# Optimization experiments

Measured on AMD Instinct MI355X. Metric: run time of the kernel, lower is better.

## Reference

```python
import jax, jax.numpy as jnp
import numpy as np

B, S, D, E, K = 4, 2048, 1024, 8, 2
LN_EPS = 1e-5


def setup_inputs() -> dict:
    key = jax.random.key(0)
    ks = jax.random.split(key, 8)
    s = 1.0 / np.sqrt(D)
    return {
        "x": jax.random.normal(ks[0], (B, S, D), dtype=jnp.float32),
        "noise": jax.random.normal(ks[1], (B, S, E), dtype=jnp.float32) * (1.0 / E),
        "W_route": jax.random.uniform(ks[2], (D, E), minval=-s, maxval=s, dtype=jnp.float32),
        "b_route": jax.random.uniform(ks[3], (E,), minval=-s, maxval=s, dtype=jnp.float32),
        "ln_gamma": jnp.ones((E,), dtype=jnp.float32),
        "ln_beta": jnp.zeros((E,), dtype=jnp.float32),
        "W_exp": jax.random.uniform(ks[4], (E, D, D), minval=-s, maxval=s, dtype=jnp.float32),
        "b_exp": jax.random.uniform(ks[5], (E, D), minval=-s, maxval=s, dtype=jnp.float32),
    }


def reference(x, noise, W_route, b_route, ln_gamma, ln_beta, W_exp, b_exp):
    # Routing: Linear(dim, E) -> LayerNorm(E) -> softmax, plus noise
    logits = jnp.einsum("bsd,de->bse", x, W_route) + b_route
    mu = logits.mean(axis=-1, keepdims=True)
    var = logits.var(axis=-1, keepdims=True)
    ln = (logits - mu) / jnp.sqrt(var + LN_EPS) * ln_gamma + ln_beta
    routing = jax.nn.softmax(ln, axis=-1) + noise

    topk_w, topk_i = jax.lax.top_k(routing, K)          # [B,S,K]
    topk_w = jax.nn.softmax(topk_w, axis=-1)

    # Dense all-expert compute (faithful to the naive original)
    expert_out = jnp.einsum("bsd,edf->bsef", x, W_exp) + b_exp  # [B,S,E,D]

    # Gather top-k experts per token and combine
    sel = jnp.take_along_axis(expert_out, topk_i[..., None], axis=2)  # [B,S,K,D]
    return (sel * topk_w[..., None]).sum(axis=2)
```

## Files before the change

### kernel.cpp

```cpp
#include <hip/hip_runtime.h>
#include <hip/hip_bf16.h>


typedef unsigned short u16;
typedef __bf16 bf16x8 __attribute__((ext_vector_type(8)));
typedef float floatx4 __attribute__((ext_vector_type(4)));
typedef unsigned short u16x8 __attribute__((ext_vector_type(8)));

#define NTOK 8192
#define DDIM 1024
#define NEXP 8

__device__ __forceinline__ u16 f2bf(float f) {
    union { float f; unsigned int i; } c; c.f = f;
    unsigned int i = c.i;
    return (u16)((i + 0x7fffu + ((i >> 16) & 1u)) >> 16);
}

__device__ __forceinline__ int swz(int row, int chunk) {
    return row * 32 + ((chunk ^ ((row >> 1) & 3)) << 3);
}

__global__ __launch_bounds__(256) void xcast(const float* __restrict__ x,
                                             u16* __restrict__ xb) {
    size_t i = ((size_t)blockIdx.x * 256 + threadIdx.x) * 8;
    float4 a = *(const float4*)(x + i);
    float4 b = *(const float4*)(x + i + 4);
    u16x8 v;
    v[0] = f2bf(a.x); v[1] = f2bf(a.y); v[2] = f2bf(a.z); v[3] = f2bf(a.w);
    v[4] = f2bf(b.x); v[5] = f2bf(b.y); v[6] = f2bf(b.z); v[7] = f2bf(b.w);
    *(u16x8*)(xb + i) = v;
}

__global__ __launch_bounds__(256) void transpose_w(const float* __restrict__ W,
                                                   u16* __restrict__ WT) {
    __shared__ __align__(16) u16 tile[64][72];
    const int e = blockIdx.z, d0 = blockIdx.y * 64, f0 = blockIdx.x * 64;
    const int t = threadIdx.x;
    const float* src = W + (size_t)e * DDIM * DDIM;
    u16* dst = WT + (size_t)e * DDIM * DDIM;
#pragma unroll
    for (int it = 0; it < 2; ++it) {
        int idx = it * 256 + t;
        int r = idx >> 3, c8 = idx & 7;
        const float* sp = src + (size_t)(d0 + r) * DDIM + f0 + c8 * 8;
        float4 va = *(const float4*)sp;
        float4 vb = *(const float4*)(sp + 4);
        u16x8 v;
        v[0] = f2bf(va.x); v[1] = f2bf(va.y); v[2] = f2bf(va.z); v[3] = f2bf(va.w);
        v[4] = f2bf(vb.x); v[5] = f2bf(vb.y); v[6] = f2bf(vb.z); v[7] = f2bf(vb.w);
        *(u16x8*)&tile[r][c8 * 8] = v;
    }
    __syncthreads();
#pragma unroll
    for (int it = 0; it < 2; ++it) {
        int idx = it * 256 + t;
        int fr = idx >> 3, d8 = idx & 7;
        u16x8 o;
#pragma unroll
        for (int j = 0; j < 8; ++j) o[j] = tile[d8 * 8 + j][fr];
        *(u16x8*)(dst + (size_t)(f0 + fr) * DDIM + d0 + d8 * 8) = o;
    }
}

__global__ __launch_bounds__(256) void routing_compute(
    const float* __restrict__ x, const float* __restrict__ noise,
    const float* __restrict__ Wr, const float* __restrict__ br,
    const float* __restrict__ gamma, const float* __restrict__ beta,
    int* __restrict__ e01, float2* __restrict__ w01) {
    __shared__ __align__(16) float wrT[NEXP][DDIM];
    const int t = threadIdx.x;
#pragma unroll
    for (int i = 0; i < 8; ++i) {
        int f4 = i * 256 + t;
        int d = f4 >> 1, half = (f4 & 1) * 4;
        float4 v = *(const float4*)&Wr[d * 8 + half];
        wrT[half + 0][d] = v.x; wrT[half + 1][d] = v.y;
        wrT[half + 2][d] = v.z; wrT[half + 3][d] = v.w;
    }
    __syncthreads();

    const int wave = t >> 6, lane = t & 63;
    const int tok = blockIdx.x * 4 + wave;
    const float4* xrow = (const float4*)(x + (size_t)tok * DDIM);
    float acc[8];
#pragma unroll
    for (int e = 0; e < 8; ++e) acc[e] = 0.f;
#pragma unroll
    for (int i = 0; i < 4; ++i) {
        int d4 = i * 64 + lane;
        float4 xv = xrow[d4];
#pragma unroll
        for (int e = 0; e < 8; ++e) {
            float4 wv = *(const float4*)&wrT[e][d4 * 4];
            acc[e] += xv.x * wv.x + xv.y * wv.y + xv.z * wv.z + xv.w * wv.w;
        }
    }
#pragma unroll
    for (int off = 32; off >= 1; off >>= 1) {
#pragma unroll
        for (int e = 0; e < 8; ++e) acc[e] += __shfl_xor(acc[e], off, 64);
    }
    if (lane == 0) {
        float lg[8], mu = 0.f;
#pragma unroll
        for (int e = 0; e < 8; ++e) { lg[e] = acc[e] + br[e]; mu += lg[e]; }
        mu *= 0.125f;
        float var = 0.f;
#pragma unroll
        for (int e = 0; e < 8; ++e) { float d = lg[e] - mu; var += d * d; }
        var *= 0.125f;
        float rstd = rsqrtf(var + 1e-5f);
        float ln[8], mx = -1e30f;
#pragma unroll
        for (int e = 0; e < 8; ++e) {
            ln[e] = (lg[e] - mu) * rstd * gamma[e] + beta[e];
            mx = fmaxf(mx, ln[e]);
        }
        float s = 0.f, p[8];
#pragma unroll
        for (int e = 0; e < 8; ++e) { p[e] = expf(ln[e] - mx); s += p[e]; }
        float inv = 1.f / s, r[8];
#pragma unroll
        for (int e = 0; e < 8; ++e) r[e] = p[e] * inv + noise[(size_t)tok * 8 + e];
        int i0 = 0; float v0 = r[0];
#pragma unroll
        for (int e = 1; e < 8; ++e) if (r[e] > v0) { v0 = r[e]; i0 = e; }
        int i1 = -1; float v1 = -1e30f;
#pragma unroll
        for (int e = 0; e < 8; ++e) if (e != i0 && r[e] > v1) { v1 = r[e]; i1 = e; }
        float w0 = 1.f / (1.f + expf(v1 - v0));
        e01[tok] = i0 | (i1 << 8);
        w01[tok] = make_float2(w0, 1.f - w0);
    }
}

__global__ __launch_bounds__(256) void build_lists(
    const int* __restrict__ e01, const float2* __restrict__ w01,
    int* __restrict__ counts, int* __restrict__ list_tok, float* __restrict__ list_w) {
    const int g = blockIdx.x;
    const int slot = g >> 3, ex = g & 7;
    const int t = threadIdx.x, wave = t >> 6, lane = t & 63;
    __shared__ int wtot[4];
    int base = 0;
    for (int start = 0; start < NTOK; start += 256) {
        int tok = start + t;
        int packed = e01[tok];
        int e = slot ? ((packed >> 8) & 0xff) : (packed & 0xff);
        bool sel = (e == ex);
        unsigned long long m = __ballot(sel);
        int prefix = __popcll(m & ((1ULL << lane) - 1ULL));
        if (lane == 0) wtot[wave] = __popcll(m);
        __syncthreads();
        int wbase = 0;
#pragma unroll
        for (int wv = 0; wv < 4; ++wv) if (wv < wave) wbase += wtot[wv];
        int total = wtot[0] + wtot[1] + wtot[2] + wtot[3];
        if (sel) {
            float2 w2 = w01[tok];
            int pos = base + wbase + prefix;
            list_tok[g * NTOK + pos] = tok;
            list_w[g * NTOK + pos] = slot ? w2.y : w2.x;
        }
        base += total;
        __syncthreads();
    }
    if (t == 0) counts[g] = base;
}

template <int BF16A>
__global__ __launch_bounds__(256) void moe_gemm(
    const float* __restrict__ xf, const u16* __restrict__ xb,
    const u16* __restrict__ WT, const float* __restrict__ bexp,
    const int* __restrict__ counts, const int* __restrict__ list_tok,
    const float* __restrict__ list_w, float* __restrict__ out,
    int grp_base, int accum) {
    const int e = blockIdx.z;
    const int grp = grp_base + e;
    int cnt = counts[grp];
    cnt = cnt < 0 ? 0 : (cnt > NTOK ? NTOK : cnt);
    const int lin = blockIdx.x;
    const int n = (lin >> 3) & 7;
    const int m = (lin & 7) | ((lin >> 6) << 3);
    const int m0 = m * 128;
    if (m0 >= cnt) return;
    const int n0 = n * 128;

    __shared__ __align__(16) u16 A_s[128 * 32];
    __shared__ __align__(16) u16 B_s[128 * 32];
    __shared__ int tok_s[128];
    __shared__ float w_s[128];
    __shared__ float bias_s[128];

    const int t = threadIdx.x;
    if (t < 128) {
        int r = m0 + t;
        int rr = r < cnt ? r : cnt - 1;
        tok_s[t] = list_tok[grp * NTOK + rr] & (NTOK - 1);
        w_s[t] = (r < cnt) ? list_w[grp * NTOK + rr] : 0.f;
        bias_s[t] = bexp[e * DDIM + n0 + t];
    }
    __syncthreads();

    const int ra = t >> 2;
    const int ch = t & 3;
    const int co = ch * 8;
    const u16* wg0 = WT + ((size_t)e * DDIM + n0 + ra) * DDIM + co;
    const u16* wg1 = WT + ((size_t)e * DDIM + n0 + 64 + ra) * DDIM + co;
    u16* sA0 = A_s + swz(ra, ch);
    u16* sA1 = A_s + swz(64 + ra, ch);
    u16* sB0 = B_s + swz(ra, ch);
    u16* sB1 = B_s + swz(64 + ra, ch);

    const int lane = t & 63, wave = t >> 6;
    const int wm = wave >> 1, wn = wave & 1;
    const int lm = lane & 15;
    const int kc = lane >> 4;

    floatx4 acc[4][4];
#pragma unroll
    for (int mi = 0; mi < 4; ++mi)
#pragma unroll
        for (int ni = 0; ni < 4; ++ni) acc[mi][ni] = (floatx4){0.f, 0.f, 0.f, 0.f};

    const float* xg0f = xf + (size_t)tok_s[ra] * DDIM + co;
    const float* xg1f = xf + (size_t)tok_s[64 + ra] * DDIM + co;
    const u16* xg0b = xb + (size_t)tok_s[ra] * DDIM + co;
    const u16* xg1b = xb + (size_t)tok_s[64 + ra] * DDIM + co;

    for (int kk = 0; kk < DDIM; kk += 32) {
        u16x8 a0, a1;
        if (BF16A) {
            a0 = *(const u16x8*)(xg0b + kk);
            a1 = *(const u16x8*)(xg1b + kk);
        } else {
            float4 fa0 = *(const float4*)(xg0f + kk);
            float4 fa0b = *(const float4*)(xg0f + kk + 4);
            float4 fa1 = *(const float4*)(xg1f + kk);
            float4 fa1b = *(const float4*)(xg1f + kk + 4);
            a0[0] = f2bf(fa0.x); a0[1] = f2bf(fa0.y); a0[2] = f2bf(fa0.z); a0[3] = f2bf(fa0.w);
            a0[4] = f2bf(fa0b.x); a0[5] = f2bf(fa0b.y); a0[6] = f2bf(fa0b.z); a0[7] = f2bf(fa0b.w);
            a1[0] = f2bf(fa1.x); a1[1] = f2bf(fa1.y); a1[2] = f2bf(fa1.z); a1[3] = f2bf(fa1.w);
            a1[4] = f2bf(fa1b.x); a1[5] = f2bf(fa1b.y); a1[6] = f2bf(fa1b.z); a1[7] = f2bf(fa1b.w);
        }
        u16x8 b0 = *(const u16x8*)(wg0 + kk);
        u16x8 b1 = *(const u16x8*)(wg1 + kk);
        __syncthreads();
        *(u16x8*)sA0 = a0;
        *(u16x8*)sA1 = a1;
        *(u16x8*)sB0 = b0;
        *(u16x8*)sB1 = b1;
        __syncthreads();
        bf16x8 af[4], bfr[4];
#pragma unroll
        for (int mi = 0; mi < 4; ++mi)
            af[mi] = *(const bf16x8*)&A_s[swz(wm * 64 + mi * 16 + lm, kc)];
#pragma unroll
        for (int ni = 0; ni < 4; ++ni)
            bfr[ni] = *(const bf16x8*)&B_s[swz(wn * 64 + ni * 16 + lm, kc)];
#pragma unroll
        for (int mi = 0; mi < 4; ++mi)
#pragma unroll
            for (int ni = 0; ni < 4; ++ni)
                acc[mi][ni] = __builtin_amdgcn_mfma_f32_16x16x32_bf16(
                    af[mi], bfr[ni], acc[mi][ni], 0, 0, 0);
    }

#pragma unroll
    for (int mi = 0; mi < 4; ++mi) {
        int rb = wm * 64 + mi * 16 + (lane >> 4) * 4;
#pragma unroll
        for (int reg = 0; reg < 4; ++reg) {
            int r = rb + reg;
            if (m0 + r < cnt) {
                size_t tok = (size_t)tok_s[r];
                float w = w_s[r];
                float* yrow = out + tok * DDIM + n0;
#pragma unroll
                for (int ni = 0; ni < 4; ++ni) {
                    int col = wn * 64 + ni * 16 + lm;
                    float v = w * (acc[mi][ni][reg] + bias_s[col]);
                    if (accum) v += yrow[col];
                    yrow[col] = v;
                }
            }
        }
    }
}

extern "C" void kernel_launch(void* const* d_in, const int* in_sizes, int n_in,
                              void* d_out, int out_size, void* d_ws, size_t ws_size,
                              hipStream_t stream) {
    const float* x     = (const float*)d_in[0];
    const float* noise = (const float*)d_in[1];
    const float* Wr    = (const float*)d_in[2];
    const float* br    = (const float*)d_in[3];
    const float* gamma = (const float*)d_in[4];
    const float* beta  = (const float*)d_in[5];
    const float* Wexp  = (const float*)d_in[6];
    const float* bexp  = (const float*)d_in[7];
    float* out = (float*)d_out;

    unsigned char* ws = (unsigned char*)d_ws;
    u16* WT       = (u16*)ws;
    int* counts   = (int*)(ws + 16777216);
    int* list_tok = (int*)(ws + 16777472);
    float* list_w = (float*)(ws + 17301760);
    int* e01      = (int*)(ws + 17826048);
    float2* w01   = (float2*)(ws + 17858816);
    u16* xb       = (u16*)(ws + 17924352);
    const size_t need_bf16a = 17924352 + 16777216;

    transpose_w<<<dim3(16, 16, 8), 256, 0, stream>>>(Wexp, WT);
    routing_compute<<<NTOK / 4, 256, 0, stream>>>(x, noise, Wr, br, gamma, beta,
                                                  e01, w01);
    build_lists<<<16, 256, 0, stream>>>(e01, w01, counts, list_tok, list_w);

    if (ws_size >= need_bf16a) {
        xcast<<<NTOK * DDIM / (256 * 8), 256, 0, stream>>>(x, xb);
        moe_gemm<1><<<dim3(512, 1, 8), 256, 0, stream>>>(
            x, xb, WT, bexp, counts, list_tok, list_w, out, 0, 0);
        moe_gemm<1><<<dim3(512, 1, 8), 256, 0, stream>>>(
            x, xb, WT, bexp, counts, list_tok, list_w, out, 8, 1);
    } else {
        moe_gemm<0><<<dim3(512, 1, 8), 256, 0, stream>>>(
            x, xb, WT, bexp, counts, list_tok, list_w, out, 0, 0);
        moe_gemm<0><<<dim3(512, 1, 8), 256, 0, stream>>>(
            x, xb, WT, bexp, counts, list_tok, list_w, out, 8, 1);
    }
}
```

Baseline: 253.4 us.

## Double K tile, prefetch next tile into registers, reorder grid, rework transpose

The MoE GEMM now uses a K step of 64 instead of 32, which halves the number of barrier pairs. The global loads for the next K tile are issued before the MFMAs of the current tile, so load latency overlaps compute. Block indexing is flattened and interleaved across experts, so the early-exit blocks for empty tiles are spread evenly. The weight transpose kernel now transposes in fp32 shared memory with padding and converts to bf16 on the way out. The costs are higher register use for the prefetch buffers and twice the LDS per block, which may reduce occupancy.

```diff
diff --git a/kernel.cpp b/kernel.cpp
--- a/kernel.cpp
+++ b/kernel.cpp
@@ -15,10 +15,6 @@
     union { float f; unsigned int i; } c; c.f = f;
     unsigned int i = c.i;
     return (u16)((i + 0x7fffu + ((i >> 16) & 1u)) >> 16);
-}
-
-__device__ __forceinline__ int swz(int row, int chunk) {
-    return row * 32 + ((chunk ^ ((row >> 1) & 3)) << 3);
 }
 
 __global__ __launch_bounds__(256) void xcast(const float* __restrict__ x,
@@ -34,33 +30,32 @@
 
 __global__ __launch_bounds__(256) void transpose_w(const float* __restrict__ W,
                                                    u16* __restrict__ WT) {
-    __shared__ __align__(16) u16 tile[64][72];
+    __shared__ float tileT[64 * 65];
     const int e = blockIdx.z, d0 = blockIdx.y * 64, f0 = blockIdx.x * 64;
     const int t = threadIdx.x;
     const float* src = W + (size_t)e * DDIM * DDIM;
     u16* dst = WT + (size_t)e * DDIM * DDIM;
-#pragma unroll
-    for (int it = 0; it < 2; ++it) {
-        int idx = it * 256 + t;
-        int r = idx >> 3, c8 = idx & 7;
-        const float* sp = src + (size_t)(d0 + r) * DDIM + f0 + c8 * 8;
-        float4 va = *(const float4*)sp;
-        float4 vb = *(const float4*)(sp + 4);
-        u16x8 v;
-        v[0] = f2bf(va.x); v[1] = f2bf(va.y); v[2] = f2bf(va.z); v[3] = f2bf(va.w);
-        v[4] = f2bf(vb.x); v[5] = f2bf(vb.y); v[6] = f2bf(vb.z); v[7] = f2bf(vb.w);
-        *(u16x8*)&tile[r][c8 * 8] = v;
+    const int r = t >> 2, q = t & 3;
+    const float* sp = src + (size_t)(d0 + r) * DDIM + f0 + q * 16;
+#pragma unroll
+    for (int j = 0; j < 4; ++j) {
+        float4 v = *(const float4*)(sp + j * 4);
+        int c = q * 16 + j * 4;
+        tileT[(c + 0) * 65 + r] = v.x;
+        tileT[(c + 1) * 65 + r] = v.y;
+        tileT[(c + 2) * 65 + r] = v.z;
+        tileT[(c + 3) * 65 + r] = v.w;
     }
     __syncthreads();
-#pragma unroll
-    for (int it = 0; it < 2; ++it) {
-        int idx = it * 256 + t;
-        int fr = idx >> 3, d8 = idx & 7;
-        u16x8 o;
-#pragma unroll
-        for (int j = 0; j < 8; ++j) o[j] = tile[d8 * 8 + j][fr];
-        *(u16x8*)(dst + (size_t)(f0 + fr) * DDIM + d0 + d8 * 8) = o;
-    }
+    const int c2 = t >> 2, dq = (t & 3) * 16;
+    u16x8 o0, o1;
+#pragma unroll
+    for (int i = 0; i < 8; ++i) o0[i] = f2bf(tileT[c2 * 65 + dq + i]);
+#pragma unroll
+    for (int i = 0; i < 8; ++i) o1[i] = f2bf(tileT[c2 * 65 + dq + 8 + i]);
+    u16* dp = dst + (size_t)(f0 + c2) * DDIM + d0 + dq;
+    *(u16x8*)dp = o0;
+    *(u16x8*)(dp + 8) = o1;
 }
 
 __global__ __launch_bounds__(256) void routing_compute(
@@ -175,19 +170,19 @@
     const int* __restrict__ counts, const int* __restrict__ list_tok,
     const float* __restrict__ list_w, float* __restrict__ out,
     int grp_base, int accum) {
-    const int e = blockIdx.z;
+    const int id = blockIdx.x;
+    const int e = id & 7;
+    const int n = (id >> 3) & 7;
+    const int m = id >> 6;
     const int grp = grp_base + e;
     int cnt = counts[grp];
     cnt = cnt < 0 ? 0 : (cnt > NTOK ? NTOK : cnt);
-    const int lin = blockIdx.x;
-    const int n = (lin >> 3) & 7;
-    const int m = (lin & 7) | ((lin >> 6) << 3);
     const int m0 = m * 128;
     if (m0 >= cnt) return;
     const int n0 = n * 128;
 
-    __shared__ __align__(16) u16 A_s[128 * 32];
-    __shared__ __align__(16) u16 B_s[128 * 32];
+    __shared__ __align__(16) u16 A_s[128 * 64];
+    __shared__ __align__(16) u16 B_s[128 * 64];
     __shared__ int tok_s[128];
     __shared__ float w_s[128];
     __shared__ float bias_s[128];
@@ -202,20 +197,25 @@
     }
     __syncthreads();
 
-    const int ra = t >> 2;
-    const int ch = t & 3;
+    const int sr = t >> 3;
+    const int ch = t & 7;
     const int co = ch * 8;
-    const u16* wg0 = WT + ((size_t)e * DDIM + n0 + ra) * DDIM + co;
-    const u16* wg1 = WT + ((size_t)e * DDIM + n0 + 64 + ra) * DDIM + co;
-    u16* sA0 = A_s + swz(ra, ch);
-    u16* sA1 = A_s + swz(64 + ra, ch);
-    u16* sB0 = B_s + swz(ra, ch);
-    u16* sB1 = B_s + swz(64 + ra, ch);
+
+    size_t arow[4];
+    u16 *adst[4], *bdst[4];
+#pragma unroll
+    for (int s = 0; s < 4; ++s) {
+        int row = s * 32 + sr;
+        arow[s] = (size_t)tok_s[row] * DDIM + co;
+        int cs = ((ch ^ (row & 7)) << 3);
+        adst[s] = A_s + row * 64 + cs;
+        bdst[s] = B_s + row * 64 + cs;
+    }
+    const u16* bsrc = WT + ((size_t)e * DDIM + n0 + sr) * DDIM + co;
 
     const int lane = t & 63, wave = t >> 6;
     const int wm = wave >> 1, wn = wave & 1;
-    const int lm = lane & 15;
-    const int kc = lane >> 4;
+    const int lm = lane & 15, kc = lane >> 4;
 
     floatx4 acc[4][4];
 #pragma unroll
@@ -223,47 +223,74 @@
 #pragma unroll
         for (int ni = 0; ni < 4; ++ni) acc[mi][ni] = (floatx4){0.f, 0.f, 0.f, 0.f};
 
-    const float* xg0f = xf + (size_t)tok_s[ra] * DDIM + co;
-    const float* xg1f = xf + (size_t)tok_s[64 + ra] * DDIM + co;
-    const u16* xg0b = xb + (size_t)tok_s[ra] * DDIM + co;
-    const u16* xg1b = xb + (size_t)tok_s[64 + ra] * DDIM + co;
-
-    for (int kk = 0; kk < DDIM; kk += 32) {
-        u16x8 a0, a1;
+    u16x8 pa[4], pb[4];
+    float4 pfa[4][2];
+#pragma unroll
+    for (int s = 0; s < 4; ++s) {
         if (BF16A) {
-            a0 = *(const u16x8*)(xg0b + kk);
-            a1 = *(const u16x8*)(xg1b + kk);
+            pa[s] = *(const u16x8*)(xb + arow[s]);
         } else {
-            float4 fa0 = *(const float4*)(xg0f + kk);
-            float4 fa0b = *(const float4*)(xg0f + kk + 4);
-            float4 fa1 = *(const float4*)(xg1f + kk);
-            float4 fa1b = *(const float4*)(xg1f + kk + 4);
-            a0[0] = f2bf(fa0.x); a0[1] = f2bf(fa0.y); a0[2] = f2bf(fa0.z); a0[3] = f2bf(fa0.w);
-            a0[4] = f2bf(fa0b.x); a0[5] = f2bf(fa0b.y); a0[6] = f2bf(fa0b.z); a0[7] = f2bf(fa0b.w);
-            a1[0] = f2bf(fa1.x); a1[1] = f2bf(fa1.y); a1[2] = f2bf(fa1.z); a1[3] = f2bf(fa1.w);
-            a1[4] = f2bf(fa1b.x); a1[5] = f2bf(fa1b.y); a1[6] = f2bf(fa1b.z); a1[7] = f2bf(fa1b.w);
-        }
-        u16x8 b0 = *(const u16x8*)(wg0 + kk);
-        u16x8 b1 = *(const u16x8*)(wg1 + kk);
+            pfa[s][0] = *(const float4*)(xf + arow[s]);
+            pfa[s][1] = *(const float4*)(xf + arow[s] + 4);
+        }
+        pb[s] = *(const u16x8*)(bsrc + (size_t)s * 32 * DDIM);
+    }
+
+    for (int kk = 0; kk < DDIM; kk += 64) {
+        u16x8 wa[4];
+#pragma unroll
+        for (int s = 0; s < 4; ++s) {
+            if (BF16A) {
+                wa[s] = pa[s];
+            } else {
+                wa[s][0] = f2bf(pfa[s][0].x); wa[s][1] = f2bf(pfa[s][0].y);
+                wa[s][2] = f2bf(pfa[s][0].z); wa[s][3] = f2bf(pfa[s][0].w);
+                wa[s][4] = f2bf(pfa[s][1].x); wa[s][5] = f2bf(pfa[s][1].y);
+                wa[s][6] = f2bf(pfa[s][1].z); wa[s][7] = f2bf(pfa[s][1].w);
+            }
+        }
         __syncthreads();
-        *(u16x8*)sA0 = a0;
-        *(u16x8*)sA1 = a1;
-        *(u16x8*)sB0 = b0;
-        *(u16x8*)sB1 = b1;
+#pragma unroll
+        for (int s = 0; s < 4; ++s) {
+            *(u16x8*)adst[s] = wa[s];
+            *(u16x8*)bdst[s] = pb[s];
+        }
         __syncthreads();
-        bf16x8 af[4], bfr[4];
-#pragma unroll
-        for (int mi = 0; mi < 4; ++mi)
-            af[mi] = *(const bf16x8*)&A_s[swz(wm * 64 + mi * 16 + lm, kc)];
-#pragma unroll
-        for (int ni = 0; ni < 4; ++ni)
-            bfr[ni] = *(const bf16x8*)&B_s[swz(wn * 64 + ni * 16 + lm, kc)];
-#pragma unroll
-        for (int mi = 0; mi < 4; ++mi)
-#pragma unroll
-            for (int ni = 0; ni < 4; ++ni)
-                acc[mi][ni] = __builtin_amdgcn_mfma_f32_16x16x32_bf16(
-                    af[mi], bfr[ni], acc[mi][ni], 0, 0, 0);
+        const int nk = kk + 64;
+        if (nk < DDIM) {
+#pragma unroll
+            for (int s = 0; s < 4; ++s) {
+                if (BF16A) {
+                    pa[s] = *(const u16x8*)(xb + arow[s] + nk);
+                } else {
+                    pfa[s][0] = *(const float4*)(xf + arow[s] + nk);
+                    pfa[s][1] = *(const float4*)(xf + arow[s] + nk + 4);
+                }
+                pb[s] = *(const u16x8*)(bsrc + (size_t)s * 32 * DDIM + nk);
+            }
+        }
+#pragma unroll
+        for (int ks = 0; ks < 2; ++ks) {
+            bf16x8 af[4], bfr[4];
+#pragma unroll
+            for (int mi = 0; mi < 4; ++mi) {
+                int row = wm * 64 + mi * 16 + lm;
+                int c = (((ks * 4 + kc) ^ (row & 7)) << 3);
+                af[mi] = *(const bf16x8*)&A_s[row * 64 + c];
+            }
+#pragma unroll
+            for (int ni = 0; ni < 4; ++ni) {
+                int row = wn * 64 + ni * 16 + lm;
+                int c = (((ks * 4 + kc) ^ (row & 7)) << 3);
+                bfr[ni] = *(const bf16x8*)&B_s[row * 64 + c];
+            }
+#pragma unroll
+            for (int mi = 0; mi < 4; ++mi)
+#pragma unroll
+                for (int ni = 0; ni < 4; ++ni)
+                    acc[mi][ni] = __builtin_amdgcn_mfma_f32_16x16x32_bf16(
+                        af[mi], bfr[ni], acc[mi][ni], 0, 0, 0);
+        }
     }
 
 #pragma unroll
@@ -318,14 +345,14 @@
 
     if (ws_size >= need_bf16a) {
         xcast<<<NTOK * DDIM / (256 * 8), 256, 0, stream>>>(x, xb);
-        moe_gemm<1><<<dim3(512, 1, 8), 256, 0, stream>>>(
+        moe_gemm<1><<<dim3(4096), 256, 0, stream>>>(
             x, xb, WT, bexp, counts, list_tok, list_w, out, 0, 0);
-        moe_gemm<1><<<dim3(512, 1, 8), 256, 0, stream>>>(
+        moe_gemm<1><<<dim3(4096), 256, 0, stream>>>(
             x, xb, WT, bexp, counts, list_tok, list_w, out, 8, 1);
     } else {
-        moe_gemm<0><<<dim3(512, 1, 8), 256, 0, stream>>>(
+        moe_gemm<0><<<dim3(4096), 256, 0, stream>>>(
             x, xb, WT, bexp, counts, list_tok, list_w, out, 0, 0);
-        moe_gemm<0><<<dim3(512, 1, 8), 256, 0, stream>>>(
+        moe_gemm<0><<<dim3(4096), 256, 0, stream>>>(
             x, xb, WT, bexp, counts, list_tok, list_w, out, 8, 1);
     }
 }
```

Measured after the change: 239.0 us. 5.7% less time.
